# Kernel optimization log

Hardware: AMD Instinct MI355X
Metric: run time of the kernel (lower is better)

The kernel has to match this reference:

```python
import jax, jax.numpy as jnp
import numpy as np

N, I, O, G = 16384, 128, 128, 16


def setup_inputs() -> dict:
    key = jax.random.key(0)
    k1, k2, k3 = jax.random.split(key, 3)
    coef_norm = np.sqrt(I) * np.sqrt(G)  # smooth_initialization=False
    return {
        "x": jax.random.normal(k1, (N, I), dtype=jnp.float32),
        "cos_amplitudes": jax.random.normal(k2, (O, I, G), dtype=jnp.float32) / coef_norm,
        "sin_amplitudes": jax.random.normal(k3, (O, I, G), dtype=jnp.float32) / coef_norm,
        "bias": jnp.zeros((O,), dtype=jnp.float32),
        "ln_gamma": jnp.ones((O,), dtype=jnp.float32),
        "ln_beta": jnp.zeros((O,), dtype=jnp.float32),
    }


def reference(x, cos_amplitudes, sin_amplitudes, bias, ln_gamma, ln_beta):
    g = cos_amplitudes.shape[-1]
    # frequencies buffer: init_freq_scale=1.0 -> [1, 2, ..., grid_size]
    freqs = jnp.arange(1, g + 1, dtype=x.dtype)  # (G,)
    phases = x[:, :, None] * freqs               # (N, I, G)
    # contraction expressed as a GEMM instead of broadcast-sum over (N,O,I,G)
    out = jnp.einsum("nig,oig->no", jnp.cos(phases), cos_amplitudes)
    out = out + jnp.einsum("nig,oig->no", jnp.sin(phases), sin_amplitudes)
    out = out + bias  # (N, O)
    # LayerNorm over output_dim, eps=1e-5 (torch default)
    mu = jnp.mean(out, axis=-1, keepdims=True)
    var = jnp.var(out, axis=-1, keepdims=True)
    out = (out - mu) / jnp.sqrt(var + 1e-5) * ln_gamma + ln_beta
    return out
```

## Files before the change

### kernel.cpp

```cpp
#include <hip/hip_runtime.h>
#include <hip/hip_bf16.h>
#include <math.h>

#define N_TOK 16384
#define I_DIM 128
#define O_DIM 128
#define G_DIM 16
#define BN 64
#define CI 4
#define KC (CI * G_DIM * 2)
#define NCHUNK (I_DIM / CI)
#define A_STRIDE 136
#define ABUF (BN * A_STRIDE)
#define BSLICE 4096
#define BBUF (4 * BSLICE)
#define C_STRIDE 132
#define PK_STRIDE 68

typedef __bf16 bf16x8 __attribute__((ext_vector_type(8)));
typedef float  f32x4  __attribute__((ext_vector_type(4)));

#define GLOAD_LDS16(g, l) __builtin_amdgcn_global_load_lds( \
    (const __attribute__((address_space(1))) void*)(g),     \
    (__attribute__((address_space(3))) void*)(l), 16, 0, 0)

__global__ __launch_bounds__(256) void fkan_pack_b(
    const float* __restrict__ cosA, const float* __restrict__ sinA,
    __bf16* __restrict__ Bp)
{
    __shared__ __align__(16) float cosL[32 * PK_STRIDE];
    __shared__ __align__(16) float sinL[32 * PK_STRIDE];
    const int b = blockIdx.x;
    const int t = threadIdx.x;
    const int c = b >> 2, cg = b & 3;

    {
        const int o_l = t >> 3;
        const int k   = t & 7;
        const float* srcc = cosA + ((size_t)(cg * 32 + o_l) * I_DIM + c * 4) * G_DIM;
        const float* srcs = sinA + ((size_t)(cg * 32 + o_l) * I_DIM + c * 4) * G_DIM;
#pragma unroll
        for (int h = 0; h < 2; ++h) {
            int col = (k + 8 * h) * 4;
            *(float4*)(cosL + o_l * PK_STRIDE + col) = *(const float4*)(srcc + col);
            *(float4*)(sinL + o_l * PK_STRIDE + col) = *(const float4*)(srcs + col);
        }
    }
    __syncthreads();

#pragma unroll
    for (int h = 0; h < 2; ++h) {
        int gi    = t + 256 * h;
        int fl    = gi >> 6;
        int lane  = gi & 63;
        int ks    = fl >> 1, ot = fl & 1;
        int row16 = lane & 15, quad = lane >> 4;
        int orow  = ot * 16 + row16;
        int colb  = ks * 16 + quad * 4;
        bf16x8 v;
#pragma unroll
        for (int j = 0; j < 4; ++j) {
            v[2 * j]     = (__bf16)cosL[orow * PK_STRIDE + colb + j];
            v[2 * j + 1] = (__bf16)sinL[orow * PK_STRIDE + colb + j];
        }
        *(bf16x8*)(Bp + ((size_t)b * 512 + gi) * 8) = v;
    }
}

__global__ __launch_bounds__(256) void fkan_main(
    const float* __restrict__ x,
    const __bf16* __restrict__ Bp,
    const float* __restrict__ bias,
    const float* __restrict__ gamma,
    const float* __restrict__ beta,
    float* __restrict__ out)
{
    __shared__ __align__(16) __bf16 smem[2 * ABUF + 2 * BBUF];
    __bf16* A0 = smem;
    __bf16* A1 = smem + ABUF;
    __bf16* B0 = smem + 2 * ABUF;
    __bf16* B1 = B0 + BBUF;

    const int t     = threadIdx.x;
    const int lane  = t & 63;
    const int cg    = t >> 6;
    const int row16 = lane & 15;
    const int quad  = lane >> 4;
    const int n0    = blockIdx.x * BN;

    const int fn  = t >> 2;
    const int fil = t & 3;

    f32x4 acc[4][2];
#pragma unroll
    for (int mt = 0; mt < 4; ++mt)
#pragma unroll
        for (int ot = 0; ot < 2; ++ot)
            acc[mt][ot] = (f32x4){0.f, 0.f, 0.f, 0.f};

    auto ld_x = [&](int c) -> float {
        return x[(size_t)(n0 + fn) * I_DIM + c * CI + fil];
    };

    auto dma_b = [&](int c, __bf16* Bw) {
        const __bf16* src = Bp + (size_t)(c * 4 + cg) * 4096 + lane * 8;
        __bf16* dst = Bw + cg * BSLICE + lane * 8;
#pragma unroll
        for (int j = 0; j < 8; ++j)
            GLOAD_LDS16(src + j * 512, dst + j * 512);
    };

    auto stage_a = [&](float xv, __bf16* Ab) {
        float s1, c1;
        __sincosf(xv, &s1, &c1);
        __align__(16) __bf16 feat[32];
        feat[0] = (__bf16)c1;
        feat[1] = (__bf16)s1;
        float ck = c1, sk = s1;
#pragma unroll
        for (int g = 1; g < 16; ++g) {
            float cn = ck * c1 - sk * s1;
            float sn = sk * c1 + ck * s1;
            feat[2 * g]     = (__bf16)cn;
            feat[2 * g + 1] = (__bf16)sn;
            ck = cn; sk = sn;
        }
        bf16x8* dst = (bf16x8*)(Ab + fn * A_STRIDE + fil * 32);
        const bf16x8* srcv = (const bf16x8*)feat;
#pragma unroll
        for (int j = 0; j < 4; ++j) dst[j] = srcv[j];
    };

    auto phase = [&](int c, const __bf16* Ar, __bf16* Aw,
                     const __bf16* Br, __bf16* Bw, float xs, float& xn) {
        int cx = (c + 2 < NCHUNK) ? c + 2 : NCHUNK - 1;
        int cb = (c + 1 < NCHUNK) ? c + 1 : NCHUNK - 1;
        xn = ld_x(cx);
        dma_b(cb, Bw);
        stage_a(xs, Aw);

        asm volatile("s_waitcnt vmcnt(9)" ::: "memory");
        __builtin_amdgcn_s_setprio(1);
#pragma unroll
        for (int ks = 0; ks < 4; ++ks) {
            bf16x8 b0 = *(const bf16x8*)(Br + cg * BSLICE + (ks * 2 + 0) * 512 + lane * 8);
            bf16x8 b1 = *(const bf16x8*)(Br + cg * BSLICE + (ks * 2 + 1) * 512 + lane * 8);
            bf16x8 a[4];
#pragma unroll
            for (int mt = 0; mt < 4; ++mt)
                a[mt] = *(const bf16x8*)(Ar + (mt * 16 + row16) * A_STRIDE
                                         + ks * 32 + quad * 8);
#pragma unroll
            for (int mt = 0; mt < 4; ++mt) {
                acc[mt][0] = __builtin_amdgcn_mfma_f32_16x16x32_bf16(a[mt], b0, acc[mt][0], 0, 0, 0);
                acc[mt][1] = __builtin_amdgcn_mfma_f32_16x16x32_bf16(a[mt], b1, acc[mt][1], 0, 0, 0);
            }
        }
        __builtin_amdgcn_s_setprio(0);

        asm volatile("s_waitcnt lgkmcnt(0)" ::: "memory");
        __builtin_amdgcn_sched_barrier(0);
        __builtin_amdgcn_s_barrier();
    };

    float xA = ld_x(0);
    float xB = ld_x(1);
    dma_b(0, B0);
    stage_a(xA, A0);
    asm volatile("s_waitcnt lgkmcnt(0)" ::: "memory");
    __builtin_amdgcn_s_barrier();

    for (int cc = 0; cc < NCHUNK / 2; ++cc) {
        phase(2 * cc,     A0, A1, B0, B1, xB, xA);
        phase(2 * cc + 1, A1, A0, B1, B0, xA, xB);
    }

    float* Cs = (float*)smem;
#pragma unroll
    for (int mt = 0; mt < 4; ++mt)
#pragma unroll
        for (int ot = 0; ot < 2; ++ot)
#pragma unroll
            for (int r = 0; r < 4; ++r)
                Cs[(mt * 16 + quad * 4 + r) * C_STRIDE + cg * 32 + ot * 16 + row16] =
                    acc[mt][ot][r];
    __syncthreads();

    {
        const int r  = t >> 2;
        const int qt = t & 3;
        const float* crow = Cs + r * C_STRIDE + qt * 32;
        float vals[32];
        float sum = 0.f, sumsq = 0.f;
#pragma unroll
        for (int j4 = 0; j4 < 8; ++j4) {
            f32x4 v4 = *(const f32x4*)(crow + 4 * j4);
#pragma unroll
            for (int e = 0; e < 4; ++e) {
                float v = v4[e] + bias[qt * 32 + 4 * j4 + e];
                vals[4 * j4 + e] = v;
                sum += v;
                sumsq += v * v;
            }
        }
        sum   += __shfl_xor(sum, 1);   sum   += __shfl_xor(sum, 2);
        sumsq += __shfl_xor(sumsq, 1); sumsq += __shfl_xor(sumsq, 2);
        float mu   = sum * (1.0f / O_DIM);
        float var  = sumsq * (1.0f / O_DIM) - mu * mu;
        float rstd = rsqrtf(var + 1e-5f);

        float* orow = out + (size_t)(n0 + r) * O_DIM + qt * 32;
#pragma unroll
        for (int j4 = 0; j4 < 8; ++j4) {
            float4 o4;
            o4.x = (vals[4*j4+0] - mu) * rstd * gamma[qt*32 + 4*j4+0] + beta[qt*32 + 4*j4+0];
            o4.y = (vals[4*j4+1] - mu) * rstd * gamma[qt*32 + 4*j4+1] + beta[qt*32 + 4*j4+1];
            o4.z = (vals[4*j4+2] - mu) * rstd * gamma[qt*32 + 4*j4+2] + beta[qt*32 + 4*j4+2];
            o4.w = (vals[4*j4+3] - mu) * rstd * gamma[qt*32 + 4*j4+3] + beta[qt*32 + 4*j4+3];
            *(float4*)(orow + 4 * j4) = o4;
        }
    }
}

extern "C" void kernel_launch(void* const* d_in, const int* in_sizes, int n_in,
                              void* d_out, int out_size, void* d_ws, size_t ws_size,
                              hipStream_t stream) {
    const float* x     = (const float*)d_in[0];
    const float* cosA  = (const float*)d_in[1];
    const float* sinA  = (const float*)d_in[2];
    const float* bias  = (const float*)d_in[3];
    const float* gamma = (const float*)d_in[4];
    const float* beta  = (const float*)d_in[5];
    float* out = (float*)d_out;

    __bf16* Bp = (__bf16*)d_ws;

    fkan_pack_b<<<dim3(128), dim3(256), 0, stream>>>(cosA, sinA, Bp);
    fkan_main<<<dim3(N_TOK / BN), dim3(256), 0, stream>>>(x, Bp, bias, gamma, beta, out);
}
```

Baseline: 117.7 us.

## Load B fragments directly into registers instead of staging through LDS

Replaces the global-to-LDS DMA of packed B tiles with direct per-lane global loads into double-buffered register arrays, removing B from shared memory and the vmcnt wait tied to the DMA. This shrinks LDS use from about 100KB to about 35KB, which can allow more resident blocks, but adds 64 VGPRs of B buffers per thread and leaves the compiler to insert waits on global loads. It also splits sincos into separate sin and cos calls and skips the redundant prefetch on the last chunk.

Result: faster. 104.6 us (-11.1%).

```diff
diff --git a/kernel.cpp b/kernel.cpp
--- a/kernel.cpp
+++ b/kernel.cpp
@@ -10,19 +10,14 @@
 #define CI 4
 #define KC (CI * G_DIM * 2)
 #define NCHUNK (I_DIM / CI)
+#define KSTEPS 4
 #define A_STRIDE 136
 #define ABUF (BN * A_STRIDE)
-#define BSLICE 4096
-#define BBUF (4 * BSLICE)
 #define C_STRIDE 132
 #define PK_STRIDE 68
 
 typedef __bf16 bf16x8 __attribute__((ext_vector_type(8)));
 typedef float  f32x4  __attribute__((ext_vector_type(4)));
-
-#define GLOAD_LDS16(g, l) __builtin_amdgcn_global_load_lds( \
-    (const __attribute__((address_space(1))) void*)(g),     \
-    (__attribute__((address_space(3))) void*)(l), 16, 0, 0)
 
 __global__ __launch_bounds__(256) void fkan_pack_b(
     const float* __restrict__ cosA, const float* __restrict__ sinA,
@@ -75,11 +70,9 @@
     const float* __restrict__ beta,
     float* __restrict__ out)
 {
-    __shared__ __align__(16) __bf16 smem[2 * ABUF + 2 * BBUF];
+    __shared__ __align__(16) __bf16 smem[2 * ABUF];
     __bf16* A0 = smem;
     __bf16* A1 = smem + ABUF;
-    __bf16* B0 = smem + 2 * ABUF;
-    __bf16* B1 = B0 + BBUF;
 
     const int t     = threadIdx.x;
     const int lane  = t & 63;
@@ -98,21 +91,24 @@
         for (int ot = 0; ot < 2; ++ot)
             acc[mt][ot] = (f32x4){0.f, 0.f, 0.f, 0.f};
 
+    bf16x8 bA[2][KSTEPS], bB[2][KSTEPS];
+
     auto ld_x = [&](int c) -> float {
         return x[(size_t)(n0 + fn) * I_DIM + c * CI + fil];
     };
 
-    auto dma_b = [&](int c, __bf16* Bw) {
-        const __bf16* src = Bp + (size_t)(c * 4 + cg) * 4096 + lane * 8;
-        __bf16* dst = Bw + cg * BSLICE + lane * 8;
-#pragma unroll
-        for (int j = 0; j < 8; ++j)
-            GLOAD_LDS16(src + j * 512, dst + j * 512);
+    auto ld_b = [&](int c, bf16x8 (&b)[2][KSTEPS]) {
+        const bf16x8* base = (const bf16x8*)Bp + ((size_t)(c * 4 + cg) * 8) * 64 + lane;
+#pragma unroll
+        for (int ks = 0; ks < KSTEPS; ++ks)
+#pragma unroll
+            for (int ot = 0; ot < 2; ++ot)
+                b[ot][ks] = base[(ks * 2 + ot) * 64];
     };
 
     auto stage_a = [&](float xv, __bf16* Ab) {
-        float s1, c1;
-        __sincosf(xv, &s1, &c1);
+        float s1 = __sinf(xv);
+        float c1 = __cosf(xv);
         __align__(16) __bf16 feat[32];
         feat[0] = (__bf16)c1;
         feat[1] = (__bf16)s1;
@@ -132,19 +128,16 @@
     };
 
     auto phase = [&](int c, const __bf16* Ar, __bf16* Aw,
-                     const __bf16* Br, __bf16* Bw, float xs, float& xn) {
-        int cx = (c + 2 < NCHUNK) ? c + 2 : NCHUNK - 1;
-        int cb = (c + 1 < NCHUNK) ? c + 1 : NCHUNK - 1;
-        xn = ld_x(cx);
-        dma_b(cb, Bw);
-        stage_a(xs, Aw);
-
-        asm volatile("s_waitcnt vmcnt(9)" ::: "memory");
+                     bf16x8 (&bcur)[2][KSTEPS], bf16x8 (&bnext)[2][KSTEPS],
+                     float xs, float& xn) {
+        const bool pf = (c + 1 < NCHUNK);
+        if (pf) ld_b(c + 1, bnext);
+        if (c + 2 < NCHUNK) xn = ld_x(c + 2);
+        if (pf) stage_a(xs, Aw);
+
         __builtin_amdgcn_s_setprio(1);
 #pragma unroll
-        for (int ks = 0; ks < 4; ++ks) {
-            bf16x8 b0 = *(const bf16x8*)(Br + cg * BSLICE + (ks * 2 + 0) * 512 + lane * 8);
-            bf16x8 b1 = *(const bf16x8*)(Br + cg * BSLICE + (ks * 2 + 1) * 512 + lane * 8);
+        for (int ks = 0; ks < KSTEPS; ++ks) {
             bf16x8 a[4];
 #pragma unroll
             for (int mt = 0; mt < 4; ++mt)
@@ -152,8 +145,8 @@
                                          + ks * 32 + quad * 8);
 #pragma unroll
             for (int mt = 0; mt < 4; ++mt) {
-                acc[mt][0] = __builtin_amdgcn_mfma_f32_16x16x32_bf16(a[mt], b0, acc[mt][0], 0, 0, 0);
-                acc[mt][1] = __builtin_amdgcn_mfma_f32_16x16x32_bf16(a[mt], b1, acc[mt][1], 0, 0, 0);
+                acc[mt][0] = __builtin_amdgcn_mfma_f32_16x16x32_bf16(a[mt], bcur[0][ks], acc[mt][0], 0, 0, 0);
+                acc[mt][1] = __builtin_amdgcn_mfma_f32_16x16x32_bf16(a[mt], bcur[1][ks], acc[mt][1], 0, 0, 0);
             }
         }
         __builtin_amdgcn_s_setprio(0);
@@ -164,15 +157,16 @@
     };
 
     float xA = ld_x(0);
-    float xB = ld_x(1);
-    dma_b(0, B0);
+    float xB;
+    ld_b(0, bA);
     stage_a(xA, A0);
+    xB = ld_x(1);
     asm volatile("s_waitcnt lgkmcnt(0)" ::: "memory");
     __builtin_amdgcn_s_barrier();
 
     for (int cc = 0; cc < NCHUNK / 2; ++cc) {
-        phase(2 * cc,     A0, A1, B0, B1, xB, xA);
-        phase(2 * cc + 1, A1, A0, B1, B0, xA, xB);
+        phase(2 * cc,     A0, A1, bA, bB, xB, xA);
+        phase(2 * cc + 1, A1, A0, bB, bA, xA, xB);
     }
 
     float* Cs = (float*)smem;
```
